# Kernel tuning notes

Hardware: AMD Instinct MI355X
Metric: run time of the kernel (lower is better)

Reference implementation:

```python
import jax, jax.numpy as jnp
import numpy as np

NUM_HEADS = 14
NUM_KV_HEADS = 2
HEAD_DIM = 64
HIDDEN = 896
ROPE_THETA = 1000000.0
NEG_INF = -1e9


def _rope_tables(seq_len, dtype=jnp.float32):
    inv_freq = 1.0 / (ROPE_THETA ** (jnp.arange(0, HEAD_DIM, 2, dtype=jnp.float32) / HEAD_DIM))
    t = jnp.arange(seq_len, dtype=jnp.float32)
    freqs = t[:, None] * inv_freq[None, :]          # [S, hd/2]
    emb = jnp.concatenate((freqs, freqs), axis=-1)  # [S, hd]
    return jnp.cos(emb).astype(dtype), jnp.sin(emb).astype(dtype)


def _rotate_half(x):
    x1, x2 = x[..., : x.shape[-1] // 2], x[..., x.shape[-1] // 2 :]
    return jnp.concatenate((-x2, x1), axis=-1)


def setup_inputs() -> dict:
    key = jax.random.key(0)
    ks = jax.random.split(key, 6)
    B, S = 2, 2048
    hidden_states = jax.random.normal(ks[0], (B, S, HIDDEN), dtype=jnp.float32)
    # additive causal mask [1, 1, S, S]
    causal = jnp.tril(jnp.ones((S, S), dtype=bool))
    attention_mask = jnp.where(causal, 0.0, NEG_INF).astype(jnp.float32)[None, None]
    sd = 1.0 / np.sqrt(HIDDEN)
    Wq = jax.random.normal(ks[1], (HIDDEN, NUM_HEADS * HEAD_DIM), dtype=jnp.float32) * sd
    bq = jnp.zeros((NUM_HEADS * HEAD_DIM,), dtype=jnp.float32)
    Wk = jax.random.normal(ks[2], (HIDDEN, NUM_KV_HEADS * HEAD_DIM), dtype=jnp.float32) * sd
    bk = jnp.zeros((NUM_KV_HEADS * HEAD_DIM,), dtype=jnp.float32)
    Wv = jax.random.normal(ks[3], (HIDDEN, NUM_KV_HEADS * HEAD_DIM), dtype=jnp.float32) * sd
    bv = jnp.zeros((NUM_KV_HEADS * HEAD_DIM,), dtype=jnp.float32)
    Wo = jax.random.normal(ks[4], (NUM_HEADS * HEAD_DIM, HIDDEN), dtype=jnp.float32) * sd
    return {
        'hidden_states': hidden_states, 'attention_mask': attention_mask,
        'Wq': Wq, 'bq': bq, 'Wk': Wk, 'bk': bk, 'Wv': Wv, 'bv': bv, 'Wo': Wo,
    }


def reference(hidden_states, attention_mask, Wq, bq, Wk, bk, Wv, bv, Wo):
    B, S, _ = hidden_states.shape
    n_groups = NUM_HEADS // NUM_KV_HEADS
    q = (hidden_states @ Wq + bq).reshape(B, S, NUM_HEADS, HEAD_DIM)
    k = (hidden_states @ Wk + bk).reshape(B, S, NUM_KV_HEADS, HEAD_DIM)
    v = (hidden_states @ Wv + bv).reshape(B, S, NUM_KV_HEADS, HEAD_DIM)

    cos, sin = _rope_tables(S, hidden_states.dtype)
    cos = cos[None, :, None, :]
    sin = sin[None, :, None, :]
    q = q * cos + _rotate_half(q) * sin
    k = k * cos + _rotate_half(k) * sin

    # GQA: repeat kv heads to match query heads
    k = jnp.repeat(k, n_groups, axis=2)  # [B, S, nH, hd]
    v = jnp.repeat(v, n_groups, axis=2)

    q = q.transpose(0, 2, 1, 3)  # [B, nH, S, hd]
    k = k.transpose(0, 2, 1, 3)
    v = v.transpose(0, 2, 1, 3)

    scores = jnp.einsum('bhqd,bhkd->bhqk', q, k) / jnp.sqrt(jnp.float32(HEAD_DIM)).astype(q.dtype)
    scores = scores + attention_mask
    attn = jax.nn.softmax(scores, axis=-1)
    out = jnp.einsum('bhqk,bhkd->bhqd', attn, v)        # [B, nH, S, hd]
    out = out.transpose(0, 2, 1, 3).reshape(B, S, -1)   # [B, S, nH*hd]
    return out @ Wo
```

## Files before the change

### kernel.cpp

```cpp
#include <hip/hip_runtime.h>
#include <hip/hip_bf16.h>
#include <math.h>

#define NH 14
#define NKV 2
#define HD 64
#define HID 896
#define SEQ 2048
#define BATCH 2

typedef __attribute__((ext_vector_type(8))) short short8;
typedef __attribute__((ext_vector_type(4))) short short4v;
typedef __attribute__((ext_vector_type(4))) float f32x4;
typedef __attribute__((ext_vector_type(4))) _Float16 half4;
typedef unsigned short ushort_t;

__device__ __forceinline__ unsigned short f2b(float f) {
    unsigned int u = __float_as_uint(f);
    unsigned int r = (u + 0x7fffu + ((u >> 16) & 1u)) >> 16;
    return (unsigned short)r;
}

__global__ __launch_bounds__(256) void xcast_kernel(
    const float* __restrict__ X, ushort_t* __restrict__ Xb)
{
    size_t i = ((size_t)blockIdx.x * 256 + threadIdx.x) * 8;
    float4 a = *(const float4*)(X + i);
    float4 b = *(const float4*)(X + i + 4);
    short8 o;
    o[0] = f2b(a.x); o[1] = f2b(a.y); o[2] = f2b(a.z); o[3] = f2b(a.w);
    o[4] = f2b(b.x); o[5] = f2b(b.y); o[6] = f2b(b.z); o[7] = f2b(b.w);
    *(short8*)(Xb + i) = o;
}

__global__ __launch_bounds__(256) void wtrans_kernel(
    const float* __restrict__ Wq, const float* __restrict__ Wk,
    const float* __restrict__ Wv, const float* __restrict__ Wo,
    ushort_t* __restrict__ WqkvT, ushort_t* __restrict__ WoT)
{
    __shared__ float tile[32][33];
    const int tx = threadIdx.x, ty = threadIdx.y;
    const int z = blockIdx.z;
    const float* src; ushort_t* dst; int N, rowoff;
    if      (z == 0) { src = Wq; dst = WqkvT; N = HID; rowoff = 0;    }
    else if (z == 1) { src = Wk; dst = WqkvT; N = 128; rowoff = 896;  }
    else if (z == 2) { src = Wv; dst = WqkvT; N = 128; rowoff = 1024; }
    else             { src = Wo; dst = WoT;   N = HID; rowoff = 0;    }
    const int k0 = blockIdx.x * 32;
    const int n0 = blockIdx.y * 32;
    if (n0 >= N) return;
    #pragma unroll
    for (int i = 0; i < 4; ++i)
        tile[ty * 4 + i][tx] = src[(size_t)(k0 + ty * 4 + i) * N + n0 + tx];
    __syncthreads();
    #pragma unroll
    for (int i = 0; i < 4; ++i)
        dst[(size_t)(rowoff + n0 + ty * 4 + i) * HID + k0 + tx]
            = f2b(tile[tx][ty * 4 + i]);
}

#define LDA 40
__global__ __launch_bounds__(256) void qkv_kernel(
    const ushort_t* __restrict__ Xb, const ushort_t* __restrict__ WqkvT,
    const float* __restrict__ bq, const float* __restrict__ bk,
    const float* __restrict__ bv,
    ushort_t* __restrict__ qbuf, ushort_t* __restrict__ kbuf,
    _Float16* __restrict__ vbuf)
{
    __shared__ ushort_t Asb[128 * LDA];
    __shared__ ushort_t Bsb[64 * LDA];
    const int tid  = threadIdx.x;
    const int w    = tid >> 6;
    const int lane = tid & 63;
    const int quad = lane >> 4;
    const int l16  = lane & 15;
    const int m0 = blockIdx.x * 128;
    const int nt = blockIdx.y;
    const int nb = nt * 64;

    f32x4 acc[2][4];
    #pragma unroll
    for (int mf = 0; mf < 2; ++mf)
        #pragma unroll
        for (int nf = 0; nf < 4; ++nf) acc[mf][nf] = (f32x4){0.f, 0.f, 0.f, 0.f};

    for (int k0 = 0; k0 < HID; k0 += 32) {
        #pragma unroll
        for (int j = 0; j < 2; ++j) {
            int u = tid + j * 256;
            int row = u >> 2, c8 = u & 3;
            *(short8*)&Asb[row * LDA + c8 * 8] =
                *(const short8*)(Xb + (size_t)(m0 + row) * HID + k0 + c8 * 8);
        }
        {
            int row = tid >> 2, c8 = tid & 3;
            *(short8*)&Bsb[row * LDA + c8 * 8] =
                *(const short8*)(WqkvT + (size_t)(nb + row) * HID + k0 + c8 * 8);
        }
        __syncthreads();
        const ushort_t* Ab = &Asb[(w * 32 + l16) * LDA + quad * 8];
        short8 a0 = *(const short8*)Ab;
        short8 a1 = *(const short8*)(Ab + 16 * LDA);
        #pragma unroll
        for (int nf = 0; nf < 4; ++nf) {
            short8 bf = *(const short8*)&Bsb[(nf * 16 + l16) * LDA + quad * 8];
            acc[0][nf] = __builtin_amdgcn_mfma_f32_16x16x32_bf16(a0, bf, acc[0][nf], 0, 0, 0);
            acc[1][nf] = __builtin_amdgcn_mfma_f32_16x16x32_bf16(a1, bf, acc[1][nf], 0, 0, 0);
        }
        __syncthreads();
    }

    float bcol[4];
    #pragma unroll
    for (int f = 0; f < 4; ++f) {
        int d = f * 16 + l16;
        bcol[f] = (nt < 14) ? bq[nt * 64 + d]
                : (nt < 16) ? bk[(nt - 14) * 64 + d]
                            : bv[(nt - 16) * 64 + d];
    }
    const float lnth = 13.815510558f;
    float if0 = expf(-((float)l16)        / 32.0f * lnth);
    float if1 = expf(-((float)(l16 + 16)) / 32.0f * lnth);

    #pragma unroll
    for (int mf = 0; mf < 2; ++mf)
        #pragma unroll
        for (int r = 0; r < 4; ++r) {
            int grow = m0 + w * 32 + mf * 16 + quad * 4 + r;
            int b = grow >> 11;
            int s = grow & 2047;
            float v0 = acc[mf][0][r] + bcol[0];
            float v1 = acc[mf][1][r] + bcol[1];
            float v2 = acc[mf][2][r] + bcol[2];
            float v3 = acc[mf][3][r] + bcol[3];
            if (nt < 16) {
                float s0, c0, s1, c1;
                sincosf((float)s * if0, &s0, &c0);
                sincosf((float)s * if1, &s1, &c1);
                float n0 = v0 * c0 - v2 * s0;
                float n2 = v2 * c0 + v0 * s0;
                float n1 = v1 * c1 - v3 * s1;
                float n3 = v3 * c1 + v1 * s1;
                v0 = n0; v1 = n1; v2 = n2; v3 = n3;
            }
            if (nt < 14) {
                ushort_t* dst = qbuf + ((size_t)(b * NH + nt) * SEQ + s) * HD;
                dst[l16]      = f2b(v0 * 0.125f);
                dst[l16 + 16] = f2b(v1 * 0.125f);
                dst[l16 + 32] = f2b(v2 * 0.125f);
                dst[l16 + 48] = f2b(v3 * 0.125f);
            } else if (nt < 16) {
                ushort_t* dst = kbuf + ((size_t)(b * NKV + nt - 14) * SEQ + s) * HD;
                dst[l16]      = f2b(v0);
                dst[l16 + 16] = f2b(v1);
                dst[l16 + 32] = f2b(v2);
                dst[l16 + 48] = f2b(v3);
            } else {
                _Float16* dst = vbuf + (size_t)(b * NKV + nt - 16) * HD * SEQ + s;
                dst[(size_t)(l16)      * SEQ] = (_Float16)v0;
                dst[(size_t)(l16 + 16) * SEQ] = (_Float16)v1;
                dst[(size_t)(l16 + 32) * SEQ] = (_Float16)v2;
                dst[(size_t)(l16 + 48) * SEQ] = (_Float16)v3;
            }
        }
}

#define LDP 72
__global__ __launch_bounds__(256) void attn_kernel(
    const ushort_t* __restrict__ qbuf, const ushort_t* __restrict__ kbuf,
    const _Float16* __restrict__ vbuf, ushort_t* __restrict__ abuf)
{
    __shared__ ushort_t Ks[64 * LDP];
    __shared__ _Float16 Vt[64 * LDP];

    const int tid  = threadIdx.x;
    const int w    = tid >> 6;
    const int lane = tid & 63;
    const int quad = lane >> 4;
    const int l16  = lane & 15;
    const int qt = 31 - blockIdx.x;
    const int h  = blockIdx.y;
    const int b  = blockIdx.z;
    const int kvh = h / (NH / NKV);
    const int myrow = w * 16 + l16;

    const ushort_t* kb_h = kbuf + (size_t)(b * NKV + kvh) * SEQ * HD;
    const _Float16* vt_h = vbuf + (size_t)(b * NKV + kvh) * HD * SEQ;

    const ushort_t* qrow =
        qbuf + ((size_t)((b * NH + h) * SEQ) + qt * 64 + myrow) * HD;
    short8 qf0 = *(const short8*)(qrow + quad * 8);
    short8 qf1 = *(const short8*)(qrow + 32 + quad * 8);

    f32x4 O[4];
    #pragma unroll
    for (int mf = 0; mf < 4; ++mf) O[mf] = (f32x4){0.f, 0.f, 0.f, 0.f};
    float m_i = -1e30f, l_i = 0.0f;

    for (int kt = 0; kt <= qt; ++kt) {
        __syncthreads();
        for (int i = tid; i < 512; i += 256) {
            int row = i >> 3, c8 = i & 7;
            *(uint4*)&Ks[row * LDP + c8 * 8] =
                *(const uint4*)(kb_h + ((size_t)(kt * 64 + row)) * HD + c8 * 8);
            *(uint4*)&Vt[row * LDP + c8 * 8] =
                *(const uint4*)(vt_h + (size_t)row * SEQ + kt * 64 + c8 * 8);
        }
        __syncthreads();

        const bool diag = (kt == qt);

        f32x4 S[4];
        #pragma unroll
        for (int f = 0; f < 4; ++f) {
            S[f] = (f32x4){0.f, 0.f, 0.f, 0.f};
            if (!diag || f <= w) {
                short8 kf0 = *(const short8*)&Ks[(f * 16 + l16) * LDP + quad * 8];
                short8 kf1 = *(const short8*)&Ks[(f * 16 + l16) * LDP + 32 + quad * 8];
                S[f] = __builtin_amdgcn_mfma_f32_16x16x32_bf16(kf0, qf0, S[f], 0, 0, 0);
                S[f] = __builtin_amdgcn_mfma_f32_16x16x32_bf16(kf1, qf1, S[f], 0, 0, 0);
            }
        }

        float sc[4][4];
        float cmax = -1e30f;
        #pragma unroll
        for (int f = 0; f < 4; ++f)
            #pragma unroll
            for (int r = 0; r < 4; ++r) {
                float v = S[f][r];
                if (diag && (f * 16 + quad * 4 + r) > myrow) v = -1e30f;
                sc[f][r] = v;
                cmax = fmaxf(cmax, v);
            }
        cmax = fmaxf(cmax, __shfl_xor(cmax, 16));
        cmax = fmaxf(cmax, __shfl_xor(cmax, 32));

        float m_new = fmaxf(m_i, cmax);
        float alpha = __expf(m_i - m_new);
        m_i = m_new;

        float psum = 0.0f;
        #pragma unroll
        for (int f = 0; f < 4; ++f)
            #pragma unroll
            for (int r = 0; r < 4; ++r) {
                float p = __expf(sc[f][r] - m_new);
                sc[f][r] = p;
                psum += p;
            }
        psum += __shfl_xor(psum, 16);
        psum += __shfl_xor(psum, 32);
        l_i = l_i * alpha + psum;

        #pragma unroll
        for (int mf = 0; mf < 4; ++mf)
            #pragma unroll
            for (int r = 0; r < 4; ++r)
                O[mf][r] *= alpha;

        half4 pb[4];
        #pragma unroll
        for (int f = 0; f < 4; ++f)
            #pragma unroll
            for (int j = 0; j < 4; ++j)
                pb[f][j] = (_Float16)sc[f][j];

        #pragma unroll
        for (int mf = 0; mf < 4; ++mf) {
            const _Float16* vb = &Vt[(mf * 16 + l16) * LDP + quad * 4];
            #pragma unroll
            for (int kc = 0; kc < 4; ++kc) {
                if (!diag || kc <= w) {
                    half4 va = *(const half4*)(vb + kc * 16);
                    O[mf] = __builtin_amdgcn_mfma_f32_16x16x16f16(va, pb[kc], O[mf], 0, 0, 0);
                }
            }
        }
    }

    float inv = 1.0f / l_i;
    ushort_t* op = abuf + (size_t)(b * SEQ + qt * 64 + myrow) * HID + h * HD;
    #pragma unroll
    for (int mf = 0; mf < 4; ++mf) {
        short4v st;
        #pragma unroll
        for (int r = 0; r < 4; ++r) st[r] = (short)f2b(O[mf][r] * inv);
        *(short4v*)(op + mf * 16 + quad * 4) = st;
    }
}

__global__ __launch_bounds__(256) void oproj_kernel(
    const ushort_t* __restrict__ A, const ushort_t* __restrict__ WoT,
    float* __restrict__ out)
{
    __shared__ ushort_t Asb[128 * LDA];
    __shared__ ushort_t Bsb[64 * LDA];
    const int tid  = threadIdx.x;
    const int w    = tid >> 6;
    const int lane = tid & 63;
    const int quad = lane >> 4;
    const int l16  = lane & 15;
    const int m0 = blockIdx.x * 128;
    const int n0 = blockIdx.y * 64;

    f32x4 acc[2][4];
    #pragma unroll
    for (int mf = 0; mf < 2; ++mf)
        #pragma unroll
        for (int nf = 0; nf < 4; ++nf) acc[mf][nf] = (f32x4){0.f, 0.f, 0.f, 0.f};

    for (int k0 = 0; k0 < HID; k0 += 32) {
        #pragma unroll
        for (int j = 0; j < 2; ++j) {
            int u = tid + j * 256;
            int row = u >> 2, c8 = u & 3;
            *(short8*)&Asb[row * LDA + c8 * 8] =
                *(const short8*)(A + (size_t)(m0 + row) * HID + k0 + c8 * 8);
        }
        {
            int row = tid >> 2, c8 = tid & 3;
            *(short8*)&Bsb[row * LDA + c8 * 8] =
                *(const short8*)(WoT + (size_t)(n0 + row) * HID + k0 + c8 * 8);
        }
        __syncthreads();
        const ushort_t* Ab = &Asb[(w * 32 + l16) * LDA + quad * 8];
        short8 a0 = *(const short8*)Ab;
        short8 a1 = *(const short8*)(Ab + 16 * LDA);
        #pragma unroll
        for (int nf = 0; nf < 4; ++nf) {
            short8 bf = *(const short8*)&Bsb[(nf * 16 + l16) * LDA + quad * 8];
            acc[0][nf] = __builtin_amdgcn_mfma_f32_16x16x32_bf16(a0, bf, acc[0][nf], 0, 0, 0);
            acc[1][nf] = __builtin_amdgcn_mfma_f32_16x16x32_bf16(a1, bf, acc[1][nf], 0, 0, 0);
        }
        __syncthreads();
    }

    #pragma unroll
    for (int mf = 0; mf < 2; ++mf)
        #pragma unroll
        for (int r = 0; r < 4; ++r) {
            size_t rbase = (size_t)(m0 + w * 32 + mf * 16 + quad * 4 + r) * HID + n0;
            #pragma unroll
            for (int f = 0; f < 4; ++f)
                out[rbase + f * 16 + l16] = acc[mf][f][r];
        }
}

extern "C" void kernel_launch(void* const* d_in, const int* in_sizes, int n_in,
                              void* d_out, int out_size, void* d_ws, size_t ws_size,
                              hipStream_t stream) {
    const float* X  = (const float*)d_in[0];
    const float* Wq = (const float*)d_in[2];
    const float* bq = (const float*)d_in[3];
    const float* Wk = (const float*)d_in[4];
    const float* bk = (const float*)d_in[5];
    const float* Wv = (const float*)d_in[6];
    const float* bv = (const float*)d_in[7];
    const float* Wo = (const float*)d_in[8];
    float* out = (float*)d_out;

    ushort_t* ws    = (ushort_t*)d_ws;
    ushort_t* Xb    = ws;
    ushort_t* WqkvT = Xb    + 3670016;
    ushort_t* WoT   = WqkvT + 1032192;
    ushort_t* qbuf  = WoT   + 802816;
    ushort_t* kbuf  = qbuf  + 3670016;
    _Float16* vbuf  = (_Float16*)(kbuf + 524288);
    ushort_t* abufb = (ushort_t*)vbuf + 524288;

    xcast_kernel<<<dim3(1792), 256, 0, stream>>>(X, Xb);
    wtrans_kernel<<<dim3(28, 28, 4), dim3(32, 8), 0, stream>>>(
        Wq, Wk, Wv, Wo, WqkvT, WoT);
    qkv_kernel<<<dim3(32, 18), 256, 0, stream>>>(
        Xb, WqkvT, bq, bk, bv, qbuf, kbuf, vbuf);
    attn_kernel<<<dim3(32, NH, BATCH), 256, 0, stream>>>(
        qbuf, kbuf, vbuf, abufb);
    oproj_kernel<<<dim3(32, 14), 256, 0, stream>>>(
        abufb, WoT, out);
}
```

Baseline: 220.0 us.

## Split attention into single-wave blocks reading K/V directly from global memory

Each attention block now has one 64-lane wave covering 16 query rows instead of four waves covering 64 rows. The shared-memory staging of K and V tiles and its two barriers per iteration are removed, and MFMA operands are loaded straight from global memory, relying on L1/L2 to serve the reuse. This gives finer-grained blocks for causal load balance and drops sync overhead. The cost is that K/V reuse across waves is lost, global traffic grows up to fourfold, and the V loads are strided 8-byte reads.

```diff
diff --git a/kernel.cpp b/kernel.cpp
--- a/kernel.cpp
+++ b/kernel.cpp
@@ -165,30 +165,26 @@
         }
 }
 
-#define LDP 72
-__global__ __launch_bounds__(256) void attn_kernel(
+__global__ __launch_bounds__(64) void attn_kernel(
     const ushort_t* __restrict__ qbuf, const ushort_t* __restrict__ kbuf,
     const _Float16* __restrict__ vbuf, ushort_t* __restrict__ abuf)
 {
-    __shared__ ushort_t Ks[64 * LDP];
-    __shared__ _Float16 Vt[64 * LDP];
-
-    const int tid  = threadIdx.x;
-    const int w    = tid >> 6;
-    const int lane = tid & 63;
+    const int lane = threadIdx.x;
     const int quad = lane >> 4;
     const int l16  = lane & 15;
-    const int qt = 31 - blockIdx.x;
+    const int g  = 127 - blockIdx.x;
     const int h  = blockIdx.y;
     const int b  = blockIdx.z;
     const int kvh = h / (NH / NKV);
-    const int myrow = w * 16 + l16;
+    const int qt  = g >> 2;
+    const int sub = g & 3;
+    const int rowl = sub * 16 + l16;
 
     const ushort_t* kb_h = kbuf + (size_t)(b * NKV + kvh) * SEQ * HD;
     const _Float16* vt_h = vbuf + (size_t)(b * NKV + kvh) * HD * SEQ;
 
     const ushort_t* qrow =
-        qbuf + ((size_t)((b * NH + h) * SEQ) + qt * 64 + myrow) * HD;
+        qbuf + ((size_t)((b * NH + h) * SEQ) + g * 16 + l16) * HD;
     short8 qf0 = *(const short8*)(qrow + quad * 8);
     short8 qf1 = *(const short8*)(qrow + 32 + quad * 8);
 
@@ -198,25 +194,18 @@
     float m_i = -1e30f, l_i = 0.0f;
 
     for (int kt = 0; kt <= qt; ++kt) {
-        __syncthreads();
-        for (int i = tid; i < 512; i += 256) {
-            int row = i >> 3, c8 = i & 7;
-            *(uint4*)&Ks[row * LDP + c8 * 8] =
-                *(const uint4*)(kb_h + ((size_t)(kt * 64 + row)) * HD + c8 * 8);
-            *(uint4*)&Vt[row * LDP + c8 * 8] =
-                *(const uint4*)(vt_h + (size_t)row * SEQ + kt * 64 + c8 * 8);
-        }
-        __syncthreads();
-
         const bool diag = (kt == qt);
+        const ushort_t* kp = kb_h + (size_t)(kt * 64) * HD;
+        const _Float16* vp = vt_h + kt * 64;
 
         f32x4 S[4];
         #pragma unroll
         for (int f = 0; f < 4; ++f) {
             S[f] = (f32x4){0.f, 0.f, 0.f, 0.f};
-            if (!diag || f <= w) {
-                short8 kf0 = *(const short8*)&Ks[(f * 16 + l16) * LDP + quad * 8];
-                short8 kf1 = *(const short8*)&Ks[(f * 16 + l16) * LDP + 32 + quad * 8];
+            if (!diag || f <= sub) {
+                const ushort_t* kr = kp + (size_t)(f * 16 + l16) * HD + quad * 8;
+                short8 kf0 = *(const short8*)kr;
+                short8 kf1 = *(const short8*)(kr + 32);
                 S[f] = __builtin_amdgcn_mfma_f32_16x16x32_bf16(kf0, qf0, S[f], 0, 0, 0);
                 S[f] = __builtin_amdgcn_mfma_f32_16x16x32_bf16(kf1, qf1, S[f], 0, 0, 0);
             }
@@ -229,7 +218,7 @@
             #pragma unroll
             for (int r = 0; r < 4; ++r) {
                 float v = S[f][r];
-                if (diag && (f * 16 + quad * 4 + r) > myrow) v = -1e30f;
+                if (diag && (f * 16 + quad * 4 + r) > rowl) v = -1e30f;
                 sc[f][r] = v;
                 cmax = fmaxf(cmax, v);
             }
@@ -268,10 +257,10 @@
 
         #pragma unroll
         for (int mf = 0; mf < 4; ++mf) {
-            const _Float16* vb = &Vt[(mf * 16 + l16) * LDP + quad * 4];
+            const _Float16* vb = vp + (size_t)(mf * 16 + l16) * SEQ + quad * 4;
             #pragma unroll
             for (int kc = 0; kc < 4; ++kc) {
-                if (!diag || kc <= w) {
+                if (!diag || kc <= sub) {
                     half4 va = *(const half4*)(vb + kc * 16);
                     O[mf] = __builtin_amdgcn_mfma_f32_16x16x16f16(va, pb[kc], O[mf], 0, 0, 0);
                 }
@@ -280,7 +269,7 @@
     }
 
     float inv = 1.0f / l_i;
-    ushort_t* op = abuf + (size_t)(b * SEQ + qt * 64 + myrow) * HID + h * HD;
+    ushort_t* op = abuf + (size_t)(b * SEQ + g * 16 + l16) * HID + h * HD;
     #pragma unroll
     for (int mf = 0; mf < 4; ++mf) {
         short4v st;
@@ -374,7 +363,7 @@
         Wq, Wk, Wv, Wo, WqkvT, WoT);
     qkv_kernel<<<dim3(32, 18), 256, 0, stream>>>(
         Xb, WqkvT, bq, bk, bv, qbuf, kbuf, vbuf);
-    attn_kernel<<<dim3(32, NH, BATCH), 256, 0, stream>>>(
+    attn_kernel<<<dim3(128, NH, BATCH), 64, 0, stream>>>(
         qbuf, kbuf, vbuf, abufb);
     oproj_kernel<<<dim3(32, 14), 256, 0, stream>>>(
         abufb, WoT, out);
```

Result: slower. 432.2 us (+96.5%).
